# Optimization experiments

Hardware: AMD Instinct MI355X
Metric: run time of the kernel (lower is better)

Reference implementation:

```python
import jax, jax.numpy as jnp
import numpy as np

B = 32       # batch
IN_N = 32    # input capsules
IN_D = 16    # input capsule dim (== out_d)
H = 14       # input spatial
OUT_N = 32   # output capsules
OUT_D = 16
HO = 7       # parent grid h_out = w_out
HID = 64     # Linformer projection dim
EPS = 1e-5


def _gconv(x, w, groups):
    # x: [b, C, H, W], w: [C_out, C_in/groups, kh, kw]; stride 1, pad 1
    return jax.lax.conv_general_dilated(
        x, w, window_strides=(1, 1), padding=((1, 1), (1, 1)),
        dimension_numbers=("NCHW", "OIHW", "NCHW"), feature_group_count=groups)


def setup_inputs() -> dict:
    key = jax.random.key(0)
    ks = jax.random.split(key, 7)
    current_pose = jax.random.normal(ks[0], (B, IN_N, H, H, IN_D), dtype=jnp.float32)
    next_pose = jax.random.normal(ks[1], (B, OUT_N, HO, HO, OUT_D), dtype=jnp.float32)
    # grouped conv weights (torch layout OIHW, groups = IN_N)
    current_w = 0.05 * jax.random.normal(ks[2], (IN_N * IN_D, IN_D, 3, 3), dtype=jnp.float32)
    next_w = 0.05 * jax.random.normal(ks[3], (OUT_N * OUT_D, OUT_N * OUT_D // IN_N, 3, 3), dtype=jnp.float32)
    E_proj = 0.02 * jax.random.normal(ks[4], (IN_N, H * H, HID), dtype=jnp.float32)
    rel_embedd = jax.random.normal(ks[5], (IN_D, HO * HO), dtype=jnp.float32)
    ln_gamma = jnp.ones((OUT_D,), dtype=jnp.float32)
    ln_beta = jnp.zeros((OUT_D,), dtype=jnp.float32)
    return {
        "current_pose": current_pose, "next_pose": next_pose,
        "current_w": current_w, "next_w": next_w,
        "E_proj": E_proj, "rel_embedd": rel_embedd,
        "ln_gamma": ln_gamma, "ln_beta": ln_beta,
        "num_iter": 1,
    }


def reference(current_pose, next_pose, current_w, next_w, E_proj, rel_embedd,
              ln_gamma, ln_beta, num_iter):
    b = current_pose.shape[0]
    # 5D -> [b, n*d, H, W]
    cp = current_pose.transpose(0, 2, 3, 1, 4).reshape(b, H, H, IN_N * IN_D)
    cp = cp.transpose(0, 3, 1, 2)
    cp = _gconv(cp, current_w, IN_N)                       # [b, n*d, H, H]
    # headwise Linformer key projection
    cp = cp.reshape(b, IN_D, IN_N, 1, H * H)
    k = jnp.matmul(cp, E_proj)                             # [b, d, n, 1, HID]
    k = k.reshape(b, IN_D, IN_N * HID).transpose(0, 2, 1)  # [b, n*HID, d]
    rel = jnp.broadcast_to(rel_embedd.T[None], (b, HO * HO, IN_D))
    k = jnp.concatenate([k, rel], axis=1)                  # [b, N, d]

    # parent pose -> queries
    q = next_pose.transpose(0, 2, 3, 1, 4).reshape(b, HO, HO, OUT_N * OUT_D)
    q = q.transpose(0, 3, 1, 2)
    q = _gconv(q, next_w, IN_N)                            # [b, out_n*out_d, HO, HO]
    q = q.reshape(b, OUT_N * HO * HO, OUT_D)               # [b, J, d]

    dots = jnp.einsum("bje,bie->bji", q, k) * (IN_D ** -0.5)  # [b, J, N]
    dots = jax.nn.softmax(dots, axis=-2)                   # softmax over queries j
    out = jnp.einsum("bji,bie->bje", dots, k)              # [b, J, d]

    out = out.reshape(b, OUT_N * IN_D, HO, HO)
    out = _gconv(out, next_w, IN_N)
    out = out.reshape(b, OUT_N, HO, HO, IN_D)

    # LayerNorm over last dim (dropout rate = 0)
    mu = out.mean(-1, keepdims=True)
    var = ((out - mu) ** 2).mean(-1, keepdims=True)
    out = (out - mu) / jnp.sqrt(var + EPS) * ln_gamma + ln_beta
    return out
```

## Files before the change

kernel.cpp:

```cpp
#include <hip/hip_runtime.h>

typedef unsigned short u16;
typedef __attribute__((ext_vector_type(8))) short short8;
typedef __attribute__((ext_vector_type(4))) float floatx4;

#define MFMA16(a, b, c) __builtin_amdgcn_mfma_f32_16x16x32_bf16(a, b, c, 0, 0, 0)

__device__ inline u16 bf16rn(float x) {
    unsigned u = __float_as_uint(x);
    u += 0x7fffu + ((u >> 16) & 1u);
    return (u16)(u >> 16);
}
__device__ inline float bf16tof(u16 h) { return __uint_as_float(((unsigned)h) << 16); }
__device__ inline short8 ld8(const u16* p) { return *(const short8*)p; }

__global__ __launch_bounds__(256) void k_conv14(const float* __restrict__ pose,
                                                const float* __restrict__ w,
                                                float* __restrict__ out) {
    int blk = blockIdx.x;
    int tid = threadIdx.x;
    __shared__ float patch[16 * 256];
#pragma unroll
    for (int k = 0; k < 16; ++k) patch[k * 256 + tid] = 0.f;
    __syncthreads();
    const float* pin = pose + (size_t)blk * 3136;
    for (int t = tid; t < 3136; t += 256) {
        int p = t >> 4, ic = t & 15;
        int y = p / 14, x = p % 14;
        patch[ic * 256 + (y + 1) * 16 + (x + 1)] = pin[t];
    }
    __syncthreads();
    int g = blk & 31;
    const float* wg = w + (size_t)g * 2304;
    float* po = out + (size_t)blk * 3136;
    if (tid < 196) {
        int y = tid / 14, x = tid % 14;
        int base = (y + 1) * 16 + (x + 1);
        float acc[16];
#pragma unroll
        for (int oc = 0; oc < 16; ++oc) acc[oc] = 0.f;
        for (int ic = 0; ic < 16; ++ic) {
            const float* pr = patch + ic * 256 + base;
            float win[9];
#pragma unroll
            for (int ky = 0; ky < 3; ++ky)
#pragma unroll
                for (int kx = 0; kx < 3; ++kx)
                    win[ky * 3 + kx] = pr[(ky - 1) * 16 + (kx - 1)];
            const float* wi = wg + ic * 9;
#pragma unroll
            for (int oc = 0; oc < 16; ++oc)
#pragma unroll
                for (int kk = 0; kk < 9; ++kk)
                    acc[oc] += win[kk] * wi[oc * 144 + kk];
        }
#pragma unroll
        for (int oc = 0; oc < 16; ++oc) po[oc * 196 + tid] = acc[oc];
    }
}

__global__ __launch_bounds__(64) void k_conv7(const float* __restrict__ in,
                                              const float* __restrict__ in2,
                                              const float* __restrict__ w,
                                              float* __restrict__ out, int mode) {
    int blk = blockIdx.x;
    int oh = blk & 1, bg = blk >> 1;
    int tid = threadIdx.x;
    __shared__ float patch[16 * 144];
    for (int t = tid; t < 16 * 144; t += 64) patch[t] = 0.f;
    __syncthreads();
    const float* pin = in + (size_t)bg * 784;
    if (mode == 1) {
        for (int t = tid; t < 784; t += 64) {
            int p = t >> 4, ic = t & 15;
            int y = p / 7, x = p % 7;
            patch[ic * 144 + (y + 1) * 16 + (x + 1)] = pin[t];
        }
    } else {
        const float* pin2 = in2 + (size_t)bg * 784;
        for (int t = tid; t < 784; t += 64) {
            int ic = t / 49, p = t % 49;
            int y = p / 7, x = p % 7;
            patch[ic * 144 + (y + 1) * 16 + (x + 1)] = pin[t] + pin2[t];
        }
    }
    __syncthreads();
    int g = bg & 31;
    const float* wg = w + (size_t)g * 2304 + (size_t)oh * 8 * 144;
    float* po = out + (size_t)bg * 784 + (size_t)oh * 8 * 49;
    if (tid < 49) {
        int y = tid / 7, x = tid % 7;
        int base = (y + 1) * 16 + (x + 1);
        float acc[8];
#pragma unroll
        for (int oc = 0; oc < 8; ++oc) acc[oc] = 0.f;
        for (int ic = 0; ic < 16; ++ic) {
            const float* pr = patch + ic * 144 + base;
            float win[9];
#pragma unroll
            for (int ky = 0; ky < 3; ++ky)
#pragma unroll
                for (int kx = 0; kx < 3; ++kx)
                    win[ky * 3 + kx] = pr[(ky - 1) * 16 + (kx - 1)];
            const float* wi = wg + ic * 9;
#pragma unroll
            for (int oc = 0; oc < 8; ++oc)
#pragma unroll
                for (int kk = 0; kk < 9; ++kk)
                    acc[oc] += win[kk] * wi[oc * 144 + kk];
        }
#pragma unroll
        for (int oc = 0; oc < 8; ++oc) po[oc * 49 + tid] = acc[oc];
    }
}

__global__ __launch_bounds__(256) void k_kproj(const float* __restrict__ cpconv,
                                               const float* __restrict__ eproj,
                                               const float* __restrict__ rel,
                                               float* __restrict__ K) {
    int blk = blockIdx.x;
    int m = blk % 33, b = blk / 33;
    int tid = threadIdx.x;
    if (m == 32) {
        for (int t = tid; t < 49 * 16; t += 256) {
            int r = t >> 4, e = t & 15;
            K[(size_t)b * (2097 * 16) + (size_t)(2048 + r) * 16 + e] = rel[e * 49 + r];
        }
        return;
    }
    __shared__ float ep[196 * 64];
    __shared__ float cr[16 * 196];
    const float* eb = eproj + (size_t)m * (196 * 64);
    for (int t = tid; t < 196 * 64; t += 256) ep[t] = eb[t];
    for (int t = tid; t < 16 * 196; t += 256) {
        int e = t / 196, p = t % 196;
        cr[t] = cpconv[(size_t)b * 100352 + (size_t)(e * 32 + m) * 196 + p];
    }
    __syncthreads();

    int e  = tid >> 4;
    int h4 = (tid & 15) * 4;
    float4 acc = {0.f, 0.f, 0.f, 0.f};
    const float* crr = cr + e * 196;
    for (int p = 0; p < 196; ++p) {
        float c = crr[p];
        float4 v = *(const float4*)(ep + p * 64 + h4);
        acc.x += c * v.x; acc.y += c * v.y; acc.z += c * v.z; acc.w += c * v.w;
    }
    size_t kb = (size_t)b * (2097 * 16) + (size_t)(m * 64 + h4) * 16 + e;
    K[kb]      = acc.x;
    K[kb + 16] = acc.y;
    K[kb + 32] = acc.z;
    K[kb + 48] = acc.w;
}

__global__ __launch_bounds__(256) void k_cvt(const float* __restrict__ qconv,
                                             const float* __restrict__ Kmat,
                                             u16* __restrict__ Qp,
                                             u16* __restrict__ Kh,
                                             u16* __restrict__ Kl,
                                             u16* __restrict__ KhT,
                                             u16* __restrict__ KlT) {
    int gid = blockIdx.x * 256 + threadIdx.x;
    if (blockIdx.x < 196) {
        const float4* q4 = (const float4*)(qconv + (size_t)gid * 16);
        float4 t0 = q4[0], t1 = q4[1], t2 = q4[2], t3 = q4[3];
        float v[16] = {t0.x,t0.y,t0.z,t0.w, t1.x,t1.y,t1.z,t1.w,
                       t2.x,t2.y,t2.z,t2.w, t3.x,t3.y,t3.z,t3.w};
        unsigned hw[8], lw[8];
#pragma unroll
        for (int t = 0; t < 8; ++t) {
            float x0 = v[2*t] * 0.25f, x1 = v[2*t+1] * 0.25f;
            u16 h0 = bf16rn(x0), h1 = bf16rn(x1);
            u16 l0 = bf16rn(x0 - bf16tof(h0)), l1 = bf16rn(x1 - bf16tof(h1));
            hw[t] = (unsigned)h0 | ((unsigned)h1 << 16);
            lw[t] = (unsigned)l0 | ((unsigned)l1 << 16);
        }
        uint4* r4 = (uint4*)(Qp + (size_t)gid * 32);
        r4[0] = make_uint4(hw[0], hw[1], hw[2], hw[3]);
        r4[1] = make_uint4(hw[4], hw[5], hw[6], hw[7]);
        r4[2] = make_uint4(lw[0], lw[1], lw[2], lw[3]);
        r4[3] = make_uint4(lw[4], lw[5], lw[6], lw[7]);
    } else {
        int id = gid - 50176;
        int b = id / 2112, i = id % 2112;
        float v[16] = {0.f};
        if (i < 2097) {
            const float4* k4 = (const float4*)(Kmat + ((size_t)b * 2097 + i) * 16);
            float4 t0 = k4[0], t1 = k4[1], t2 = k4[2], t3 = k4[3];
            v[0]=t0.x; v[1]=t0.y; v[2]=t0.z; v[3]=t0.w;
            v[4]=t1.x; v[5]=t1.y; v[6]=t1.z; v[7]=t1.w;
            v[8]=t2.x; v[9]=t2.y; v[10]=t2.z; v[11]=t2.w;
            v[12]=t3.x; v[13]=t3.y; v[14]=t3.z; v[15]=t3.w;
        }
        u16 hi[16], lo[16];
#pragma unroll
        for (int e = 0; e < 16; ++e) {
            hi[e] = bf16rn(v[e]);
            lo[e] = bf16rn(v[e] - bf16tof(hi[e]));
        }
        unsigned hw[8], lw[8];
#pragma unroll
        for (int t = 0; t < 8; ++t) {
            hw[t] = (unsigned)hi[2*t] | ((unsigned)hi[2*t+1] << 16);
            lw[t] = (unsigned)lo[2*t] | ((unsigned)lo[2*t+1] << 16);
        }
        uint4* kh4 = (uint4*)(Kh + (size_t)id * 16);
        uint4* kl4 = (uint4*)(Kl + (size_t)id * 16);
        kh4[0] = make_uint4(hw[0], hw[1], hw[2], hw[3]);
        kh4[1] = make_uint4(hw[4], hw[5], hw[6], hw[7]);
        kl4[0] = make_uint4(lw[0], lw[1], lw[2], lw[3]);
        kl4[1] = make_uint4(lw[4], lw[5], lw[6], lw[7]);
        size_t tb = (size_t)b * 33792 + i;
#pragma unroll
        for (int e = 0; e < 16; ++e) {
            KhT[tb + e * 2112] = hi[e];
            KlT[tb + e * 2112] = lo[e];
        }
    }
}

__global__ __launch_bounds__(256) void k_stats3(const u16* __restrict__ Qp,
                                                const u16* __restrict__ Kh,
                                                const u16* __restrict__ Kl,
                                                float* __restrict__ dpart) {
    __shared__ __align__(16) u16 ql[2][640];
    int blk = blockIdx.x;
    int b = blk / 66; int r2 = blk % 66; int jh = r2 / 33; int itb = r2 % 33;
    int tid = threadIdx.x, wave = tid >> 6, lane = tid & 63;
    int n = lane & 15, quad = lane >> 4;
    int it = itb * 4 + wave;
    int ibase = it * 16;
    size_t krow = ((size_t)b * 2112 + ibase + n) * 16 + (quad & 1) * 8;
    short8 bh = ld8(Kh + krow);
    short8 bl = ld8(Kl + krow);
    int jt0 = jh * 49;
    const u16* Qb = Qp + (size_t)b * 50176;
    uint4 sreg;
    auto ldc = [&](int c) {
        if (tid < 64) sreg = *(const uint4*)(Qb + (size_t)(jt0 + c) * 512 + (tid >> 2) * 32 + (tid & 3) * 8);
    };
    auto stc = [&](int buf) {
        if (tid < 64) *(uint4*)(&ql[buf][(tid >> 2) * 40 + (tid & 3) * 8]) = sreg;
    };
    floatx4 dacc = {0.f, 0.f, 0.f, 0.f};
    ldc(0); stc(0); ldc(1);
    __syncthreads();
    for (int c = 0; c < 49; ++c) {
        if (c + 1 < 49) stc((c + 1) & 1);
        if (c + 2 < 49) ldc(c + 2);
        short8 a = ld8(&ql[c & 1][n * 40 + quad * 8]);
        floatx4 s = {0.f, 0.f, 0.f, 0.f};
        s = MFMA16(a, bh, s);
        s = MFMA16(a, bl, s);
        dacc.x += __expf(s.x); dacc.y += __expf(s.y);
        dacc.z += __expf(s.z); dacc.w += __expf(s.w);
        __syncthreads();
    }
    float d = dacc.x + dacc.y + dacc.z + dacc.w;
    d += __shfl_xor(d, 16);
    d += __shfl_xor(d, 32);
    if (quad == 0) dpart[(size_t)jh * 67584 + (size_t)b * 2112 + ibase + n] = d;
}

__global__ __launch_bounds__(256) void k_pv3(const u16* __restrict__ Qp,
                                             const u16* __restrict__ Kh,
                                             const u16* __restrict__ Kl,
                                             const u16* __restrict__ KhT,
                                             const u16* __restrict__ KlT,
                                             const float* __restrict__ dpart,
                                             float* __restrict__ opart) {
    __shared__ __align__(16) u16 khl[2][768], kll[2][768];
    __shared__ __align__(16) u16 khtl[2][640], kltl[2][640];
    __shared__ __align__(16) u16 wt[4][2][640];
    __shared__ float rll[2][32];

    int blk = blockIdx.x;
    int b = blk / 50; int rem = blk % 50; int jtb = rem >> 1; int ih = rem & 1;
    int tid = threadIdx.x, wave = tid >> 6, lane = tid & 63;
    int n = lane & 15, quad = lane >> 4;
    int jt = jtb * 4 + wave;
    int jtc = jt < 98 ? jt : 97;
    int i0 = ih * 1056;
    size_t bK = (size_t)b * 2112;
    size_t bT = (size_t)b * 33792;
    const float* d0p = dpart + bK;
    const float* d1p = dpart + 67584 + bK;

    short8 aq = ld8(Qp + ((size_t)b * 1568 + (size_t)jtc * 16 + n) * 32 + quad * 8);

    int role = tid >> 6, rt = tid & 63;
    uint4 sreg; float da = 0.f, db = 0.f;
    auto ldchunk = [&](int c) {
        int i0c = i0 + c * 32;
        if (role == 0)      sreg = *(const uint4*)(Kh  + (bK + i0c + (rt >> 1)) * 16 + (rt & 1) * 8);
        else if (role == 1) sreg = *(const uint4*)(Kl  + (bK + i0c + (rt >> 1)) * 16 + (rt & 1) * 8);
        else if (role == 2) sreg = *(const uint4*)(KhT + bT + (size_t)(rt >> 2) * 2112 + i0c + (rt & 3) * 8);
        else                sreg = *(const uint4*)(KlT + bT + (size_t)(rt >> 2) * 2112 + i0c + (rt & 3) * 8);
        if (tid < 32) { da = d0p[i0c + tid]; db = d1p[i0c + tid]; }
    };
    auto stchunk = [&](int buf) {
        if (role == 0)      *(uint4*)(&khl[buf][(rt >> 1) * 24 + (rt & 1) * 8]) = sreg;
        else if (role == 1) *(uint4*)(&kll[buf][(rt >> 1) * 24 + (rt & 1) * 8]) = sreg;
        else if (role == 2) *(uint4*)(&khtl[buf][(rt >> 2) * 40 + (rt & 3) * 8]) = sreg;
        else                *(uint4*)(&kltl[buf][(rt >> 2) * 40 + (rt & 3) * 8]) = sreg;
        if (tid < 32) rll[buf][tid] = 1.0f / (da + db);
    };

    floatx4 o = {0.f, 0.f, 0.f, 0.f};
    u16* wh = &wt[wave][0][0];
    u16* wl = &wt[wave][1][0];

    ldchunk(0); stchunk(0); ldchunk(1);
    __syncthreads();
    for (int c = 0; c < 33; ++c) {
        if (c + 1 < 33) stchunk((c + 1) & 1);
        if (c + 2 < 33) ldchunk(c + 2);
        const u16* khb = &khl[c & 1][0];
        const u16* klb = &kll[c & 1][0];
        const u16* thb = &khtl[c & 1][0];
        const u16* tlb = &kltl[c & 1][0];
        short8 sh0 = ld8(khb + n * 24 + (quad & 1) * 8);
        short8 sh1 = ld8(khb + (16 + n) * 24 + (quad & 1) * 8);
        short8 sl0 = ld8(klb + n * 24 + (quad & 1) * 8);
        short8 sl1 = ld8(klb + (16 + n) * 24 + (quad & 1) * 8);
        short8 th  = ld8(thb + n * 40 + quad * 8);
        short8 tl  = ld8(tlb + n * 40 + quad * 8);
        float rl0 = rll[c & 1][n], rl1 = rll[c & 1][n + 16];
        floatx4 s0 = {0.f, 0.f, 0.f, 0.f};
        s0 = MFMA16(aq, sh0, s0);
        s0 = MFMA16(aq, sl0, s0);
        floatx4 s1 = {0.f, 0.f, 0.f, 0.f};
        s1 = MFMA16(aq, sh1, s1);
        s1 = MFMA16(aq, sl1, s1);
#pragma unroll
        for (int r = 0; r < 4; ++r) {
            float w0 = __expf(s0[r]) * rl0;
            float w1 = __expf(s1[r]) * rl1;
            unsigned u0 = __float_as_uint(w0), u1 = __float_as_uint(w1);
            float l0 = w0 - __uint_as_float(u0 & 0xffff0000u);
            float l1 = w1 - __uint_as_float(u1 & 0xffff0000u);
            int row = (quad * 4 + r) * 40;
            wh[row + n]      = (u16)(u0 >> 16);
            wh[row + 16 + n] = (u16)(u1 >> 16);
            wl[row + n]      = (u16)(__float_as_uint(l0) >> 16);
            wl[row + 16 + n] = (u16)(__float_as_uint(l1) >> 16);
        }
        asm volatile("s_waitcnt lgkmcnt(0)" ::: "memory");
        short8 awh = ld8(wh + n * 40 + quad * 8);
        short8 awl = ld8(wl + n * 40 + quad * 8);
        o = MFMA16(awh, th, o);
        o = MFMA16(awh, tl, o);
        o = MFMA16(awl, th, o);
        __syncthreads();
    }
    if (jt < 98) {
        float* ob = opart + (size_t)ih * 802816 + ((size_t)b * 1568 + (size_t)jt * 16) * 16;
#pragma unroll
        for (int r = 0; r < 4; ++r) ob[(quad * 4 + r) * 16 + n] = o[r];
    }
}

__global__ __launch_bounds__(256) void k_ln(const float* __restrict__ x,
                                            const float* __restrict__ gamma,
                                            const float* __restrict__ beta,
                                            float* __restrict__ out, int ngroups) {
    int g = blockIdx.x * 256 + threadIdx.x;
    if (g >= ngroups) return;
    const float4* xp = (const float4*)(x + (size_t)g * 16);
    float4 x0 = xp[0], x1 = xp[1], x2 = xp[2], x3 = xp[3];
    float sum = x0.x + x0.y + x0.z + x0.w + x1.x + x1.y + x1.z + x1.w
              + x2.x + x2.y + x2.z + x2.w + x3.x + x3.y + x3.z + x3.w;
    float mu = sum * 0.0625f;
    float var = 0.f;
    var += (x0.x-mu)*(x0.x-mu) + (x0.y-mu)*(x0.y-mu) + (x0.z-mu)*(x0.z-mu) + (x0.w-mu)*(x0.w-mu);
    var += (x1.x-mu)*(x1.x-mu) + (x1.y-mu)*(x1.y-mu) + (x1.z-mu)*(x1.z-mu) + (x1.w-mu)*(x1.w-mu);
    var += (x2.x-mu)*(x2.x-mu) + (x2.y-mu)*(x2.y-mu) + (x2.z-mu)*(x2.z-mu) + (x2.w-mu)*(x2.w-mu);
    var += (x3.x-mu)*(x3.x-mu) + (x3.y-mu)*(x3.y-mu) + (x3.z-mu)*(x3.z-mu) + (x3.w-mu)*(x3.w-mu);
    float rstd = rsqrtf(var * 0.0625f + 1e-5f);
    const float4* gp = (const float4*)gamma;
    const float4* bp = (const float4*)beta;
    float4 g0 = gp[0], g1 = gp[1], g2 = gp[2], g3 = gp[3];
    float4 be0 = bp[0], be1 = bp[1], be2 = bp[2], be3 = bp[3];
    float4 o0, o1, o2, o3;
    o0.x = (x0.x-mu)*rstd*g0.x + be0.x; o0.y = (x0.y-mu)*rstd*g0.y + be0.y;
    o0.z = (x0.z-mu)*rstd*g0.z + be0.z; o0.w = (x0.w-mu)*rstd*g0.w + be0.w;
    o1.x = (x1.x-mu)*rstd*g1.x + be1.x; o1.y = (x1.y-mu)*rstd*g1.y + be1.y;
    o1.z = (x1.z-mu)*rstd*g1.z + be1.z; o1.w = (x1.w-mu)*rstd*g1.w + be1.w;
    o2.x = (x2.x-mu)*rstd*g2.x + be2.x; o2.y = (x2.y-mu)*rstd*g2.y + be2.y;
    o2.z = (x2.z-mu)*rstd*g2.z + be2.z; o2.w = (x2.w-mu)*rstd*g2.w + be2.w;
    o3.x = (x3.x-mu)*rstd*g3.x + be3.x; o3.y = (x3.y-mu)*rstd*g3.y + be3.y;
    o3.z = (x3.z-mu)*rstd*g3.z + be3.z; o3.w = (x3.w-mu)*rstd*g3.w + be3.w;
    float4* op = (float4*)(out + (size_t)g * 16);
    op[0] = o0; op[1] = o1; op[2] = o2; op[3] = o3;
}

extern "C" void kernel_launch(void* const* d_in, const int* in_sizes, int n_in,
                              void* d_out, int out_size, void* d_ws, size_t ws_size,
                              hipStream_t stream) {
    const float* current_pose = (const float*)d_in[0];
    const float* next_pose    = (const float*)d_in[1];
    const float* current_w    = (const float*)d_in[2];
    const float* next_w       = (const float*)d_in[3];
    const float* E_proj       = (const float*)d_in[4];
    const float* rel          = (const float*)d_in[5];
    const float* ln_gamma     = (const float*)d_in[6];
    const float* ln_beta      = (const float*)d_in[7];
    float* out = (float*)d_out;
    float* ws  = (float*)d_ws;

    float* cpconv = ws;
    float* conv2  = ws;
    float* opart  = ws + 802816;
    float* dpart  = ws + 2408448;
    float* qconv  = ws + 3211264;
    float* Kmat   = ws + 4014080;
    u16*   ub     = (u16*)(ws + 5087744);
    u16* Qp  = ub;
    u16* Kh  = ub + 1605632;
    u16* Kl  = ub + 2686976;
    u16* KhT = ub + 3768320;
    u16* KlT = ub + 4849664;

    k_conv14<<<1024, 256, 0, stream>>>(current_pose, current_w, cpconv);
    k_conv7 <<<2048, 64,  0, stream>>>(next_pose, next_pose, next_w, qconv, 1);
    k_kproj <<<1056, 256, 0, stream>>>(cpconv, E_proj, rel, Kmat);
    k_cvt   <<<460,  256, 0, stream>>>(qconv, Kmat, Qp, Kh, Kl, KhT, KlT);
    k_stats3<<<2112, 256, 0, stream>>>(Qp, Kh, Kl, dpart);
    k_pv3   <<<1600, 256, 0, stream>>>(Qp, Kh, Kl, KhT, KlT, dpart, opart);
    k_conv7 <<<2048, 64,  0, stream>>>(opart, opart + 802816, next_w, conv2, 0);
    k_ln    <<<196,  256, 0, stream>>>(conv2, ln_gamma, ln_beta, out, 50176);
}
```

Baseline: 261.5 us.

## Move Linformer key projection to split-bf16 MFMA and restructure stats/PV kernels

The fp32 LDS-based key projection is replaced by a split-bf16 MFMA GEMM. A new kernel pre-converts E_proj into transposed hi/lo bf16, and the projection writes K in bf16 hi/lo and transposed forms directly, so the fp32 K intermediate and its conversion pass go away. The stats kernel drops LDS staging and barriers: each wave handles 32 keys and reads queries from global with register prefetch. The PV kernel packs hi/lo weights into one 32-bit LDS word, pre-sums the denominators, and moves the next-chunk store and load after the MFMAs. Risks include the precision of the split-bf16 projection and more global traffic in the stats kernel.

```diff
diff --git a/kernel.cpp b/kernel.cpp
--- a/kernel.cpp
+++ b/kernel.cpp
@@ -114,55 +114,101 @@
     }
 }
 
-__global__ __launch_bounds__(256) void k_kproj(const float* __restrict__ cpconv,
-                                               const float* __restrict__ eproj,
-                                               const float* __restrict__ rel,
-                                               float* __restrict__ K) {
+__global__ __launch_bounds__(256) void k_ecvt(const float* __restrict__ E,
+                                              u16* __restrict__ EhT,
+                                              u16* __restrict__ ElT) {
+    __shared__ float ep[196 * 65];
+    int m = blockIdx.x, tid = threadIdx.x;
+    const float* eb = E + (size_t)m * 12544;
+    for (int t = tid; t < 12544; t += 256) {
+        int p = t >> 6, h = t & 63;
+        ep[p * 65 + h] = eb[t];
+    }
+    __syncthreads();
+    for (int t = tid; t < 64 * 224; t += 256) {
+        int h = t / 224, p = t % 224;
+        float v = (p < 196) ? ep[p * 65 + h] : 0.f;
+        u16 hi = bf16rn(v);
+        u16 lo = bf16rn(v - bf16tof(hi));
+        EhT[(size_t)m * 14336 + t] = hi;
+        ElT[(size_t)m * 14336 + t] = lo;
+    }
+}
+
+__global__ __launch_bounds__(256) void k_kproj2(const float* __restrict__ cpconv,
+                                                const u16* __restrict__ EhT,
+                                                const u16* __restrict__ ElT,
+                                                u16* __restrict__ Kh,
+                                                u16* __restrict__ Kl,
+                                                u16* __restrict__ KhT,
+                                                u16* __restrict__ KlT) {
     int blk = blockIdx.x;
-    int m = blk % 33, b = blk / 33;
-    int tid = threadIdx.x;
-    if (m == 32) {
-        for (int t = tid; t < 49 * 16; t += 256) {
-            int r = t >> 4, e = t & 15;
-            K[(size_t)b * (2097 * 16) + (size_t)(2048 + r) * 16 + e] = rel[e * 49 + r];
-        }
-        return;
-    }
-    __shared__ float ep[196 * 64];
-    __shared__ float cr[16 * 196];
-    const float* eb = eproj + (size_t)m * (196 * 64);
-    for (int t = tid; t < 196 * 64; t += 256) ep[t] = eb[t];
-    for (int t = tid; t < 16 * 196; t += 256) {
-        int e = t / 196, p = t % 196;
-        cr[t] = cpconv[(size_t)b * 100352 + (size_t)(e * 32 + m) * 196 + p];
-    }
-    __syncthreads();
-
-    int e  = tid >> 4;
-    int h4 = (tid & 15) * 4;
-    float4 acc = {0.f, 0.f, 0.f, 0.f};
-    const float* crr = cr + e * 196;
-    for (int p = 0; p < 196; ++p) {
-        float c = crr[p];
-        float4 v = *(const float4*)(ep + p * 64 + h4);
-        acc.x += c * v.x; acc.y += c * v.y; acc.z += c * v.z; acc.w += c * v.w;
-    }
-    size_t kb = (size_t)b * (2097 * 16) + (size_t)(m * 64 + h4) * 16 + e;
-    K[kb]      = acc.x;
-    K[kb + 16] = acc.y;
-    K[kb + 32] = acc.z;
-    K[kb + 48] = acc.w;
+    int b = blk >> 5, m = blk & 31;
+    int wave = threadIdx.x >> 6, lane = threadIdx.x & 63;
+    int ht = wave;
+    int n = lane & 15, quad = lane >> 4;
+
+    const float* arow = cpconv + ((size_t)b * 512 + (size_t)n * 32 + m) * 196;
+    const u16* bhrow = EhT + ((size_t)m * 64 + ht * 16 + n) * 224;
+    const u16* blrow = ElT + ((size_t)m * 64 + ht * 16 + n) * 224;
+
+    floatx4 c = {0.f, 0.f, 0.f, 0.f};
+#pragma unroll
+    for (int pc = 0; pc < 7; ++pc) {
+        int p0 = pc * 32 + quad * 8;
+        float av[8];
+        if (p0 <= 188) {
+            float4 x = *(const float4*)(arow + p0);
+            float4 y = *(const float4*)(arow + p0 + 4);
+            av[0]=x.x; av[1]=x.y; av[2]=x.z; av[3]=x.w;
+            av[4]=y.x; av[5]=y.y; av[6]=y.z; av[7]=y.w;
+        } else {
+#pragma unroll
+            for (int k2 = 0; k2 < 8; ++k2) av[k2] = (p0 + k2 < 196) ? arow[p0 + k2] : 0.f;
+        }
+        short8 ah, al;
+#pragma unroll
+        for (int k2 = 0; k2 < 8; ++k2) {
+            u16 h = bf16rn(av[k2]);
+            ah[k2] = (short)h;
+            al[k2] = (short)bf16rn(av[k2] - bf16tof(h));
+        }
+        short8 bh = ld8(bhrow + pc * 32 + quad * 8);
+        short8 bl = ld8(blrow + pc * 32 + quad * 8);
+        c = MFMA16(ah, bh, c);
+        c = MFMA16(ah, bl, c);
+        c = MFMA16(al, bh, c);
+    }
+    int i = m * 64 + ht * 16 + n;
+    size_t bK = (size_t)b * 2112;
+    size_t bT = (size_t)b * 33792;
+    u16 h[4], l[4];
+#pragma unroll
+    for (int r = 0; r < 4; ++r) {
+        h[r] = bf16rn(c[r]);
+        l[r] = bf16rn(c[r] - bf16tof(h[r]));
+    }
+    *(uint2*)(Kh + (bK + i) * 16 + quad * 4) =
+        make_uint2((unsigned)h[0] | ((unsigned)h[1] << 16), (unsigned)h[2] | ((unsigned)h[3] << 16));
+    *(uint2*)(Kl + (bK + i) * 16 + quad * 4) =
+        make_uint2((unsigned)l[0] | ((unsigned)l[1] << 16), (unsigned)l[2] | ((unsigned)l[3] << 16));
+#pragma unroll
+    for (int r = 0; r < 4; ++r) {
+        KhT[bT + (size_t)(quad * 4 + r) * 2112 + i] = h[r];
+        KlT[bT + (size_t)(quad * 4 + r) * 2112 + i] = l[r];
+    }
 }
 
 __global__ __launch_bounds__(256) void k_cvt(const float* __restrict__ qconv,
-                                             const float* __restrict__ Kmat,
+                                             const float* __restrict__ rel,
                                              u16* __restrict__ Qp,
                                              u16* __restrict__ Kh,
                                              u16* __restrict__ Kl,
                                              u16* __restrict__ KhT,
                                              u16* __restrict__ KlT) {
-    int gid = blockIdx.x * 256 + threadIdx.x;
-    if (blockIdx.x < 196) {
+    int blk = blockIdx.x, tid = threadIdx.x;
+    if (blk < 196) {
+        int gid = blk * 256 + tid;
         const float4* q4 = (const float4*)(qconv + (size_t)gid * 16);
         float4 t0 = q4[0], t1 = q4[1], t2 = q4[2], t3 = q4[3];
         float v[16] = {t0.x,t0.y,t0.z,t0.w, t1.x,t1.y,t1.z,t1.w,
@@ -182,103 +228,85 @@
         r4[2] = make_uint4(lw[0], lw[1], lw[2], lw[3]);
         r4[3] = make_uint4(lw[4], lw[5], lw[6], lw[7]);
     } else {
-        int id = gid - 50176;
-        int b = id / 2112, i = id % 2112;
-        float v[16] = {0.f};
-        if (i < 2097) {
-            const float4* k4 = (const float4*)(Kmat + ((size_t)b * 2097 + i) * 16);
-            float4 t0 = k4[0], t1 = k4[1], t2 = k4[2], t3 = k4[3];
-            v[0]=t0.x; v[1]=t0.y; v[2]=t0.z; v[3]=t0.w;
-            v[4]=t1.x; v[5]=t1.y; v[6]=t1.z; v[7]=t1.w;
-            v[8]=t2.x; v[9]=t2.y; v[10]=t2.z; v[11]=t2.w;
-            v[12]=t3.x; v[13]=t3.y; v[14]=t3.z; v[15]=t3.w;
-        }
-        u16 hi[16], lo[16];
-#pragma unroll
-        for (int e = 0; e < 16; ++e) {
-            hi[e] = bf16rn(v[e]);
-            lo[e] = bf16rn(v[e] - bf16tof(hi[e]));
-        }
-        unsigned hw[8], lw[8];
-#pragma unroll
-        for (int t = 0; t < 8; ++t) {
-            hw[t] = (unsigned)hi[2*t] | ((unsigned)hi[2*t+1] << 16);
-            lw[t] = (unsigned)lo[2*t] | ((unsigned)lo[2*t+1] << 16);
-        }
-        uint4* kh4 = (uint4*)(Kh + (size_t)id * 16);
-        uint4* kl4 = (uint4*)(Kl + (size_t)id * 16);
-        kh4[0] = make_uint4(hw[0], hw[1], hw[2], hw[3]);
-        kh4[1] = make_uint4(hw[4], hw[5], hw[6], hw[7]);
-        kl4[0] = make_uint4(lw[0], lw[1], lw[2], lw[3]);
-        kl4[1] = make_uint4(lw[4], lw[5], lw[6], lw[7]);
-        size_t tb = (size_t)b * 33792 + i;
-#pragma unroll
-        for (int e = 0; e < 16; ++e) {
-            KhT[tb + e * 2112] = hi[e];
-            KlT[tb + e * 2112] = lo[e];
-        }
-    }
-}
-
-__global__ __launch_bounds__(256) void k_stats3(const u16* __restrict__ Qp,
+        int b = blk - 196;
+        size_t bK = (size_t)b * 2112;
+        size_t bT = (size_t)b * 33792;
+#pragma unroll
+        for (int k = 0; k < 4; ++k) {
+            int idx = tid + k * 256;
+            int row = idx >> 4, e = idx & 15;
+            int i = 2048 + row;
+            float v = (row < 49) ? rel[e * 49 + row] : 0.f;
+            u16 h = bf16rn(v);
+            u16 l = bf16rn(v - bf16tof(h));
+            Kh[(bK + i) * 16 + e] = h;
+            Kl[(bK + i) * 16 + e] = l;
+            KhT[bT + (size_t)e * 2112 + i] = h;
+            KlT[bT + (size_t)e * 2112 + i] = l;
+        }
+    }
+}
+
+__global__ __launch_bounds__(256) void k_stats4(const u16* __restrict__ Qp,
                                                 const u16* __restrict__ Kh,
                                                 const u16* __restrict__ Kl,
                                                 float* __restrict__ dpart) {
-    __shared__ __align__(16) u16 ql[2][640];
     int blk = blockIdx.x;
-    int b = blk / 66; int r2 = blk % 66; int jh = r2 / 33; int itb = r2 % 33;
-    int tid = threadIdx.x, wave = tid >> 6, lane = tid & 63;
+    int b = blk / 34; int rem = blk % 34; int jh = rem / 17; int tb = rem % 17;
+    int wave = threadIdx.x >> 6, lane = threadIdx.x & 63;
+    int it2 = tb * 4 + wave;
+    if (it2 >= 66) return;
+    int ibase = it2 * 32;
     int n = lane & 15, quad = lane >> 4;
-    int it = itb * 4 + wave;
-    int ibase = it * 16;
-    size_t krow = ((size_t)b * 2112 + ibase + n) * 16 + (quad & 1) * 8;
-    short8 bh = ld8(Kh + krow);
-    short8 bl = ld8(Kl + krow);
-    int jt0 = jh * 49;
-    const u16* Qb = Qp + (size_t)b * 50176;
-    uint4 sreg;
-    auto ldc = [&](int c) {
-        if (tid < 64) sreg = *(const uint4*)(Qb + (size_t)(jt0 + c) * 512 + (tid >> 2) * 32 + (tid & 3) * 8);
-    };
-    auto stc = [&](int buf) {
-        if (tid < 64) *(uint4*)(&ql[buf][(tid >> 2) * 40 + (tid & 3) * 8]) = sreg;
-    };
-    floatx4 dacc = {0.f, 0.f, 0.f, 0.f};
-    ldc(0); stc(0); ldc(1);
-    __syncthreads();
+    size_t bK = (size_t)b * 2112;
+    const u16* kb = Kh + (bK + ibase + n) * 16 + (quad & 1) * 8;
+    const u16* lb = Kl + (bK + ibase + n) * 16 + (quad & 1) * 8;
+    short8 bh0 = ld8(kb), bh1 = ld8(kb + 256);
+    short8 bl0 = ld8(lb), bl1 = ld8(lb + 256);
+    const u16* qb = Qp + (size_t)b * 50176 + (size_t)jh * 49 * 512 + n * 32 + quad * 8;
+    floatx4 d0 = {0.f,0.f,0.f,0.f}, d1 = {0.f,0.f,0.f,0.f};
+    short8 a0 = ld8(qb), a1 = ld8(qb + 512);
     for (int c = 0; c < 49; ++c) {
-        if (c + 1 < 49) stc((c + 1) & 1);
-        if (c + 2 < 49) ldc(c + 2);
-        short8 a = ld8(&ql[c & 1][n * 40 + quad * 8]);
-        floatx4 s = {0.f, 0.f, 0.f, 0.f};
-        s = MFMA16(a, bh, s);
-        s = MFMA16(a, bl, s);
-        dacc.x += __expf(s.x); dacc.y += __expf(s.y);
-        dacc.z += __expf(s.z); dacc.w += __expf(s.w);
-        __syncthreads();
-    }
-    float d = dacc.x + dacc.y + dacc.z + dacc.w;
-    d += __shfl_xor(d, 16);
-    d += __shfl_xor(d, 32);
-    if (quad == 0) dpart[(size_t)jh * 67584 + (size_t)b * 2112 + ibase + n] = d;
-}
-
-__global__ __launch_bounds__(256) void k_pv3(const u16* __restrict__ Qp,
+        short8 a2 = (c + 2 < 49) ? ld8(qb + (size_t)(c + 2) * 512) : a0;
+        floatx4 s0 = {0.f,0.f,0.f,0.f}, s1 = {0.f,0.f,0.f,0.f};
+        s0 = MFMA16(a0, bh0, s0);
+        s0 = MFMA16(a0, bl0, s0);
+        s1 = MFMA16(a0, bh1, s1);
+        s1 = MFMA16(a0, bl1, s1);
+        d0.x += __expf(s0.x); d0.y += __expf(s0.y);
+        d0.z += __expf(s0.z); d0.w += __expf(s0.w);
+        d1.x += __expf(s1.x); d1.y += __expf(s1.y);
+        d1.z += __expf(s1.z); d1.w += __expf(s1.w);
+        a0 = a1; a1 = a2;
+    }
+    float t0 = d0.x + d0.y + d0.z + d0.w;
+    float t1 = d1.x + d1.y + d1.z + d1.w;
+    t0 += __shfl_xor(t0, 16); t0 += __shfl_xor(t0, 32);
+    t1 += __shfl_xor(t1, 16); t1 += __shfl_xor(t1, 32);
+    if (quad == 0) {
+        dpart[(size_t)jh * 67584 + bK + ibase + n]      = t0;
+        dpart[(size_t)jh * 67584 + bK + ibase + 16 + n] = t1;
+    }
+}
+
+__global__ __launch_bounds__(256) void k_pv4(const u16* __restrict__ Qp,
                                              const u16* __restrict__ Kh,
                                              const u16* __restrict__ Kl,
                                              const u16* __restrict__ KhT,
                                              const u16* __restrict__ KlT,
                                              const float* __restrict__ dpart,
                                              float* __restrict__ opart) {
-    __shared__ __align__(16) u16 khl[2][768], kll[2][768];
-    __shared__ __align__(16) u16 khtl[2][640], kltl[2][640];
-    __shared__ __align__(16) u16 wt[4][2][640];
+    __shared__ __align__(16) u16 sH[2][32][2][8];
+    __shared__ __align__(16) u16 sL[2][32][2][8];
+    __shared__ __align__(16) u16 tH[2][16][32];
+    __shared__ __align__(16) u16 tL[2][16][32];
+    __shared__ __align__(16) unsigned wbuf[4][16][36];
     __shared__ float rll[2][32];
 
     int blk = blockIdx.x;
     int b = blk / 50; int rem = blk % 50; int jtb = rem >> 1; int ih = rem & 1;
     int tid = threadIdx.x, wave = tid >> 6, lane = tid & 63;
-    int n = lane & 15, quad = lane >> 4;
+    int n = lane & 15, quad = lane >> 4, qh = quad & 1;
     int jt = jtb * 4 + wave;
     int jtc = jt < 98 ? jt : 97;
     int i0 = ih * 1056;
@@ -289,69 +317,75 @@
 
     short8 aq = ld8(Qp + ((size_t)b * 1568 + (size_t)jtc * 16 + n) * 32 + quad * 8);
 
-    int role = tid >> 6, rt = tid & 63;
-    uint4 sreg; float da = 0.f, db = 0.f;
+    int role = wave, L = lane;
+    uint4 sreg; float dv = 1.f;
     auto ldchunk = [&](int c) {
         int i0c = i0 + c * 32;
-        if (role == 0)      sreg = *(const uint4*)(Kh  + (bK + i0c + (rt >> 1)) * 16 + (rt & 1) * 8);
-        else if (role == 1) sreg = *(const uint4*)(Kl  + (bK + i0c + (rt >> 1)) * 16 + (rt & 1) * 8);
-        else if (role == 2) sreg = *(const uint4*)(KhT + bT + (size_t)(rt >> 2) * 2112 + i0c + (rt & 3) * 8);
-        else                sreg = *(const uint4*)(KlT + bT + (size_t)(rt >> 2) * 2112 + i0c + (rt & 3) * 8);
-        if (tid < 32) { da = d0p[i0c + tid]; db = d1p[i0c + tid]; }
+        if (role == 0)      sreg = *(const uint4*)(Kh  + (bK + i0c + (L >> 1)) * 16 + (L & 1) * 8);
+        else if (role == 1) sreg = *(const uint4*)(Kl  + (bK + i0c + (L >> 1)) * 16 + (L & 1) * 8);
+        else if (role == 2) sreg = *(const uint4*)(KhT + bT + (size_t)(L >> 2) * 2112 + i0c + (L & 3) * 8);
+        else {
+            sreg = *(const uint4*)(KlT + bT + (size_t)(L >> 2) * 2112 + i0c + (L & 3) * 8);
+            if (L < 32) dv = d0p[i0c + L] + d1p[i0c + L];
+        }
     };
-    auto stchunk = [&](int buf) {
-        if (role == 0)      *(uint4*)(&khl[buf][(rt >> 1) * 24 + (rt & 1) * 8]) = sreg;
-        else if (role == 1) *(uint4*)(&kll[buf][(rt >> 1) * 24 + (rt & 1) * 8]) = sreg;
-        else if (role == 2) *(uint4*)(&khtl[buf][(rt >> 2) * 40 + (rt & 3) * 8]) = sreg;
-        else                *(uint4*)(&kltl[buf][(rt >> 2) * 40 + (rt & 3) * 8]) = sreg;
-        if (tid < 32) rll[buf][tid] = 1.0f / (da + db);
+    auto stchunk = [&](int bf) {
+        if (role == 0)      *(uint4*)(&sH[bf][L >> 1][L & 1][0]) = sreg;
+        else if (role == 1) *(uint4*)(&sL[bf][L >> 1][L & 1][0]) = sreg;
+        else if (role == 2) *(uint4*)(&tH[bf][L >> 2][(L & 3) * 8]) = sreg;
+        else {
+            *(uint4*)(&tL[bf][L >> 2][(L & 3) * 8]) = sreg;
+            if (L < 32) rll[bf][L] = 1.0f / dv;
+        }
     };
 
     floatx4 o = {0.f, 0.f, 0.f, 0.f};
-    u16* wh = &wt[wave][0][0];
-    u16* wl = &wt[wave][1][0];
 
     ldchunk(0); stchunk(0); ldchunk(1);
     __syncthreads();
     for (int c = 0; c < 33; ++c) {
-        if (c + 1 < 33) stchunk((c + 1) & 1);
-        if (c + 2 < 33) ldchunk(c + 2);
-        const u16* khb = &khl[c & 1][0];
-        const u16* klb = &kll[c & 1][0];
-        const u16* thb = &khtl[c & 1][0];
-        const u16* tlb = &kltl[c & 1][0];
-        short8 sh0 = ld8(khb + n * 24 + (quad & 1) * 8);
-        short8 sh1 = ld8(khb + (16 + n) * 24 + (quad & 1) * 8);
-        short8 sl0 = ld8(klb + n * 24 + (quad & 1) * 8);
-        short8 sl1 = ld8(klb + (16 + n) * 24 + (quad & 1) * 8);
-        short8 th  = ld8(thb + n * 40 + quad * 8);
-        short8 tl  = ld8(tlb + n * 40 + quad * 8);
-        float rl0 = rll[c & 1][n], rl1 = rll[c & 1][n + 16];
-        floatx4 s0 = {0.f, 0.f, 0.f, 0.f};
+        int cb = c & 1;
+        short8 sh0 = ld8(&sH[cb][n][qh][0]);
+        short8 sh1 = ld8(&sH[cb][16 + n][qh][0]);
+        short8 sl0 = ld8(&sL[cb][n][qh][0]);
+        short8 sl1 = ld8(&sL[cb][16 + n][qh][0]);
+        short8 th  = ld8(&tH[cb][n][quad * 8]);
+        short8 tl  = ld8(&tL[cb][n][quad * 8]);
+        float r0 = rll[cb][n], r1 = rll[cb][16 + n];
+        floatx4 s0 = {0.f,0.f,0.f,0.f};
         s0 = MFMA16(aq, sh0, s0);
         s0 = MFMA16(aq, sl0, s0);
-        floatx4 s1 = {0.f, 0.f, 0.f, 0.f};
+        floatx4 s1 = {0.f,0.f,0.f,0.f};
         s1 = MFMA16(aq, sh1, s1);
         s1 = MFMA16(aq, sl1, s1);
 #pragma unroll
         for (int r = 0; r < 4; ++r) {
-            float w0 = __expf(s0[r]) * rl0;
-            float w1 = __expf(s1[r]) * rl1;
+            float w0 = __expf(s0[r]) * r0;
+            float w1 = __expf(s1[r]) * r1;
             unsigned u0 = __float_as_uint(w0), u1 = __float_as_uint(w1);
-            float l0 = w0 - __uint_as_float(u0 & 0xffff0000u);
-            float l1 = w1 - __uint_as_float(u1 & 0xffff0000u);
-            int row = (quad * 4 + r) * 40;
-            wh[row + n]      = (u16)(u0 >> 16);
-            wh[row + 16 + n] = (u16)(u1 >> 16);
-            wl[row + n]      = (u16)(__float_as_uint(l0) >> 16);
-            wl[row + 16 + n] = (u16)(__float_as_uint(l1) >> 16);
+            unsigned h0 = u0 & 0xffff0000u, h1 = u1 & 0xffff0000u;
+            float l0 = w0 - __uint_as_float(h0);
+            float l1 = w1 - __uint_as_float(h1);
+            wbuf[wave][quad * 4 + r][n]      = h0 | (__float_as_uint(l0) >> 16);
+            wbuf[wave][quad * 4 + r][16 + n] = h1 | (__float_as_uint(l1) >> 16);
         }
         asm volatile("s_waitcnt lgkmcnt(0)" ::: "memory");
-        short8 awh = ld8(wh + n * 40 + quad * 8);
-        short8 awl = ld8(wl + n * 40 + quad * 8);
-        o = MFMA16(awh, th, o);
-        o = MFMA16(awh, tl, o);
-        o = MFMA16(awl, th, o);
+        uint4 wa = *(const uint4*)(&wbuf[wave][n][quad * 8]);
+        uint4 wb = *(const uint4*)(&wbuf[wave][n][quad * 8 + 4]);
+        union { unsigned u[4]; short8 s; } hv, lv;
+        hv.u[0] = (wa.x >> 16) | (wa.y & 0xffff0000u);
+        hv.u[1] = (wa.z >> 16) | (wa.w & 0xffff0000u);
+        hv.u[2] = (wb.x >> 16) | (wb.y & 0xffff0000u);
+        hv.u[3] = (wb.z >> 16) | (wb.w & 0xffff0000u);
+        lv.u[0] = (wa.x & 0xffffu) | (wa.y << 16);
+        lv.u[1] = (wa.z & 0xffffu) | (wa.w << 16);
+        lv.u[2] = (wb.x & 0xffffu) | (wb.y << 16);
+        lv.u[3] = (wb.z & 0xffffu) | (wb.w << 16);
+        o = MFMA16(hv.s, th, o);
+        o = MFMA16(hv.s, tl, o);
+        o = MFMA16(lv.s, th, o);
+        if (c < 32) stchunk((c + 1) & 1);
+        if (c < 31) ldchunk(c + 2);
         __syncthreads();
     }
     if (jt < 98) {
@@ -414,20 +448,22 @@
     float* opart  = ws + 802816;
     float* dpart  = ws + 2408448;
     float* qconv  = ws + 3211264;
-    float* Kmat   = ws + 4014080;
-    u16*   ub     = (u16*)(ws + 5087744);
+    u16*   ub     = (u16*)(ws + 4014080);
     u16* Qp  = ub;
     u16* Kh  = ub + 1605632;
     u16* Kl  = ub + 2686976;
     u16* KhT = ub + 3768320;
     u16* KlT = ub + 4849664;
+    u16* EhT = ub + 5931008;
+    u16* ElT = ub + 6389760;
 
     k_conv14<<<1024, 256, 0, stream>>>(current_pose, current_w, cpconv);
     k_conv7 <<<2048, 64,  0, stream>>>(next_pose, next_pose, next_w, qconv, 1);
-    k_kproj <<<1056, 256, 0, stream>>>(cpconv, E_proj, rel, Kmat);
-    k_cvt   <<<460,  256, 0, stream>>>(qconv, Kmat, Qp, Kh, Kl, KhT, KlT);
-    k_stats3<<<2112, 256, 0, stream>>>(Qp, Kh, Kl, dpart);
-    k_pv3   <<<1600, 256, 0, stream>>>(Qp, Kh, Kl, KhT, KlT, dpart, opart);
+    k_ecvt  <<<32,   256, 0, stream>>>(E_proj, EhT, ElT);
+    k_cvt   <<<228,  256, 0, stream>>>(qconv, rel, Qp, Kh, Kl, KhT, KlT);
+    k_kproj2<<<1024, 256, 0, stream>>>(cpconv, EhT, ElT, Kh, Kl, KhT, KlT);
+    k_stats4<<<1088, 256, 0, stream>>>(Qp, Kh, Kl, dpart);
+    k_pv4   <<<1600, 256, 0, stream>>>(Qp, Kh, Kl, KhT, KlT, dpart, opart);
     k_conv7 <<<2048, 64,  0, stream>>>(opart, opart + 802816, next_w, conv2, 0);
     k_ln    <<<196,  256, 0, stream>>>(conv2, ln_gamma, ln_beta, out, 50176);
 }
```

Measured after the change: 245.0 us. 1.07x faster.
